# Optimization experiments

Hardware: AMD Instinct MI355X
Metric: run time of the kernel (lower is better)

## Reference

```python
import jax, jax.numpy as jnp
import numpy as np

TOP_K = 3
THRESH = 0.2
# scales=[1] -> multi_scale_fft reduces to one full-length window:
# combined_amplitudes = |rfft(x, axis=1)|.mean(channels)

def setup_inputs() -> dict:
    key = jax.random.key(0)
    x = jax.random.normal(key, (64, 4096, 64), dtype=jnp.float32)
    return {"x": x}

def _autocorr_score(xi, p):
    # xi: [T, C]; p: scalar int32 period (guaranteed in [2, T//2]).
    # Equivalent to mean over consecutive period-segments i of
    # cosine_similarity(flatten(seg_i), flatten(seg_{i+1})) — computed via
    # prefix sums of lag-p cross products so the segment reshape never needs
    # a data-dependent shape.
    T, C = xi.shape
    t = jnp.arange(T)
    tp = t + p
    m = (tp < T).astype(xi.dtype)
    xs = xi[jnp.clip(tp, 0, T - 1)]                  # [T, C] rows shifted by p
    r = (xi * xs).sum(-1) * m                        # <x[t], x[t+p]>
    q = (xi * xi).sum(-1)                            # ||x[t]||^2
    z = jnp.zeros((1,), xi.dtype)
    CR = jnp.concatenate([z, jnp.cumsum(r)])         # [T+1]
    CQ = jnp.concatenate([z, jnp.cumsum(q)])
    nper = T // p
    i = jnp.arange(T // 2)                           # max possible segments (p>=2)
    seg = i < (nper - 1)
    s = jnp.clip(i * p, 0, T)
    e = jnp.clip((i + 1) * p, 0, T)
    e2 = jnp.clip((i + 2) * p, 0, T)
    dots = CR[e] - CR[s]                             # flat dot(seg_i, seg_{i+1})
    na = jnp.sqrt(jnp.maximum(CQ[e] - CQ[s], 0.0))
    nb = jnp.sqrt(jnp.maximum(CQ[e2] - CQ[e], 0.0))
    cos = dots / jnp.maximum(na * nb, 1e-8)          # F.cosine_similarity eps
    denom = jnp.maximum(nper - 1, 1).astype(xi.dtype)
    score = jnp.where(seg, cos, 0.0).sum() / denom
    return jnp.where(nper >= 2, score, 0.0)

def reference(x):
    B, T, C = x.shape
    half = T // 2
    # multi-scale FFT with scales=[1]: single window == full sequence
    amps = jnp.abs(jnp.fft.rfft(x, axis=1)).mean(-1)       # [B, T//2+1]
    _, idx = jax.lax.top_k(amps, 2 * TOP_K)                 # [B, 2K]
    period_f = T / (idx + 1).astype(jnp.float32)            # candidate periods
    in_range = (period_f >= 2.0) & (period_f <= half)       # float-period filter
    p_int = jnp.clip(jnp.floor(period_f).astype(jnp.int32), 2, half)
    pf_floor = jnp.floor(period_f)
    in_range_int = (pf_floor >= 2.0) & (pf_floor <= half)   # int-period filter
    # autocorrelation validation score per (batch, candidate)
    scores = jax.vmap(lambda xi, ps: jax.vmap(lambda p: _autocorr_score(xi, p))(ps))(x, p_int)  # [B, 2K]
    valid = in_range & in_range_int & (scores > THRESH)
    # deterministic fallback periods (torch.randint branch unreachable for TOP_K=3)
    common = np.array([T // 4, T // 3, T // 2, int(T / 1.5)], dtype=np.int32)
    common = common[(common >= 2) & (common <= half)]
    add = jnp.asarray(common)                               # [>= TOP_K]

    def select(p_row, v_row):
        order = jnp.argsort(jnp.logical_not(v_row), stable=True)  # valid first, order kept
        sp = p_row[order][:TOP_K]
        cnt = jnp.minimum(v_row.sum(), TOP_K)
        j = jnp.arange(TOP_K)
        filled = jnp.where(j < cnt, sp, add[jnp.clip(j - cnt, 0, add.shape[0] - 1)])
        w = jnp.where(j < cnt, 1.0, 0.5)
        return filled.astype(jnp.float32), w.astype(jnp.float32)

    periods, weights = jax.vmap(select)(p_int, valid)       # [B, TOP_K] each
    return periods, weights
```

## Files before the change

### kernel.cpp

```cpp
#include <hip/hip_runtime.h>
#include <math.h>

#define T_LEN 4096
#define C_CH 64
#define B_N 64
#define NBINS 2049
#define K2 6
#define TOPK 3
#define THRESH_V 0.2f

#define PIDX(i) ((i) + ((i) >> 5))
#define ZSZ (T_LEN + (T_LEN >> 5))

__device__ __forceinline__ unsigned short f2bf(float v) {
    unsigned int u = __float_as_uint(v);
    u += 0x7FFFu + ((u >> 16) & 1u);
    return (unsigned short)(u >> 16);
}
__device__ __forceinline__ float bf2f(unsigned short h) {
    return __uint_as_float(((unsigned int)h) << 16);
}
__device__ __forceinline__ float2 zld(unsigned int v) {
    return make_float2(__uint_as_float(v << 16), __uint_as_float(v & 0xFFFF0000u));
}
__device__ __forceinline__ unsigned int zst(float2 z) {
    return (unsigned int)f2bf(z.x) | ((unsigned int)f2bf(z.y) << 16);
}

__device__ __forceinline__ float2 cmul(float2 a, float2 b) {
    return make_float2(a.x * b.x - a.y * b.y, a.x * b.y + a.y * b.x);
}
__device__ __forceinline__ float2 cadd(float2 a, float2 b) { return make_float2(a.x + b.x, a.y + b.y); }
__device__ __forceinline__ float2 csub(float2 a, float2 b) { return make_float2(a.x - b.x, a.y - b.y); }

__device__ __forceinline__ void dft16(float2* v) {
    const float C2 = 0.70710678118654752f;
    const float C1 = 0.92387953251128676f;
    const float S1 = 0.38268343236508977f;
    const int br[16] = {0, 8, 4, 12, 2, 10, 6, 14, 1, 9, 5, 13, 3, 11, 7, 15};
    float2 a[16];
#pragma unroll
    for (int i = 0; i < 16; ++i) a[i] = v[br[i]];
#pragma unroll
    for (int g = 0; g < 16; g += 2) {
        float2 t = a[g + 1];
        a[g + 1] = csub(a[g], t);
        a[g] = cadd(a[g], t);
    }
#pragma unroll
    for (int g = 0; g < 16; g += 4) {
        {
            float2 t = a[g + 2];
            a[g + 2] = csub(a[g], t);
            a[g] = cadd(a[g], t);
        }
        {
            float2 t = make_float2(a[g + 3].y, -a[g + 3].x);
            a[g + 3] = csub(a[g + 1], t);
            a[g + 1] = cadd(a[g + 1], t);
        }
    }
    {
        const float2 W4[4] = {{1.f, 0.f}, {C2, -C2}, {0.f, -1.f}, {-C2, -C2}};
#pragma unroll
        for (int g = 0; g < 16; g += 8)
#pragma unroll
            for (int j = 0; j < 4; ++j) {
                float2 t = cmul(W4[j], a[g + 4 + j]);
                a[g + 4 + j] = csub(a[g + j], t);
                a[g + j] = cadd(a[g + j], t);
            }
    }
    {
        const float2 W8[8] = {{1.f, 0.f}, {C1, -S1}, {C2, -C2}, {S1, -C1},
                              {0.f, -1.f}, {-S1, -C1}, {-C2, -C2}, {-C1, -S1}};
#pragma unroll
        for (int j = 0; j < 8; ++j) {
            float2 t = cmul(W8[j], a[8 + j]);
            a[8 + j] = csub(a[j], t);
            a[j] = cadd(a[j], t);
        }
    }
#pragma unroll
    for (int i = 0; i < 16; ++i) v[i] = a[i];
}

__global__ void transpose_cvt_kernel(const float* __restrict__ x,
                                     unsigned short* __restrict__ xtbf,
                                     float* __restrict__ amps) {
    __shared__ float tile[64][65];
    const int b = blockIdx.y;
    const int t0 = blockIdx.x * 64;
    const int lane = threadIdx.x & 63;
    const int w = threadIdx.x >> 6;
    {
        const int blin = blockIdx.y * (T_LEN / 64) + blockIdx.x;
        if (threadIdx.x < 34) {
            int idx = blin * 34 + threadIdx.x;
            if (idx < B_N * NBINS) amps[idx] = 0.f;
        }
    }
    const float* xb = x + (size_t)b * T_LEN * C_CH;
#pragma unroll
    for (int i = 0; i < 16; ++i) {
        int r = w * 16 + i;
        tile[r][lane] = xb[(size_t)(t0 + r) * C_CH + lane];
    }
    __syncthreads();
    const int half = lane >> 5;
    const int tc = (lane & 31) * 2;
#pragma unroll
    for (int it = 0; it < 8; ++it) {
        int c = it * 8 + w * 2 + half;
        float v0 = tile[tc][c];
        float v1 = tile[tc + 1][c];
        unsigned int o = (unsigned int)f2bf(v0) | ((unsigned int)f2bf(v1) << 16);
        unsigned int* dst = (unsigned int*)(xtbf + ((size_t)b * C_CH + c) * T_LEN + t0);
        dst[lane & 31] = o;
    }
}

template <int MODE>
__launch_bounds__(256, 8)
__global__ void fft_amp_kernel(const void* __restrict__ srcv, float* __restrict__ amps) {
    __shared__ unsigned int Z[ZSZ];
    const int pair = blockIdx.x;
    const int b = blockIdx.y;
    const int tid = threadIdx.x;

    if (MODE == 0) {
        const unsigned short* r0 =
            (const unsigned short*)srcv + ((size_t)b * C_CH + pair * 2) * T_LEN;
        const unsigned short* r1 = r0 + T_LEN;
#pragma unroll
        for (int k = 0; k < 2; ++k) {
            int t0 = k * 2048 + tid * 8;
            uint4 u0 = *(const uint4*)(r0 + t0);
            uint4 u1 = *(const uint4*)(r1 + t0);
            unsigned int a[4] = {u0.x, u0.y, u0.z, u0.w};
            unsigned int c[4] = {u1.x, u1.y, u1.z, u1.w};
#pragma unroll
            for (int j = 0; j < 4; ++j) {
                Z[PIDX(t0 + 2 * j)] = (a[j] & 0xFFFFu) | (c[j] << 16);
                Z[PIDX(t0 + 2 * j + 1)] = (a[j] >> 16) | (c[j] & 0xFFFF0000u);
            }
        }
    } else {
        const float* x = (const float*)srcv;
        const int c0 = pair * 2;
        for (int t = tid; t < T_LEN; t += 256) {
            float2 v = *(const float2*)(x + ((size_t)b * T_LEN + t) * C_CH + c0);
            Z[PIDX(t)] = zst(v);
        }
    }
    __syncthreads();

    {
        float2 v[16];
#pragma unroll
        for (int t = 0; t < 16; ++t) v[t] = zld(Z[PIDX(tid + 256 * t)]);
        dft16(v);
        float s, c;
        __sincosf(-(float)tid * 1.5339807878856412e-3f, &s, &c);
        float2 w1 = make_float2(c, s), w = w1;
#pragma unroll
        for (int r = 1; r < 16; ++r) {
            v[r] = cmul(v[r], w);
            w = cmul(w, w1);
        }
#pragma unroll
        for (int r = 0; r < 16; ++r) Z[PIDX(256 * r + tid)] = zst(v[r]);
    }
    __syncthreads();

    {
        const int r = tid >> 4, mu = tid & 15;
        float2 v[16];
#pragma unroll
        for (int nu = 0; nu < 16; ++nu) v[nu] = zld(Z[PIDX(256 * r + mu + 16 * nu)]);
        dft16(v);
        float s, c;
        __sincosf(-(float)mu * 2.4543692606170259e-2f, &s, &c);
        float2 w1 = make_float2(c, s), w = w1;
#pragma unroll
        for (int rho = 1; rho < 16; ++rho) {
            v[rho] = cmul(v[rho], w);
            w = cmul(w, w1);
        }
#pragma unroll
        for (int rho = 0; rho < 16; ++rho) Z[PIDX(256 * r + mu + 16 * rho)] = zst(v[rho]);
    }
    __builtin_amdgcn_wave_barrier();

    {
        const int r = tid >> 4, rho = tid & 15;
        float2 v[16];
#pragma unroll
        for (int mu = 0; mu < 16; ++mu) v[mu] = zld(Z[PIDX(256 * r + mu + 16 * rho)]);
        dft16(v);
#pragma unroll
        for (int mp = 0; mp < 16; ++mp) Z[PIDX(256 * r + mp + 16 * rho)] = zst(v[mp]);
    }
    __syncthreads();

    for (int k = tid; k < NBINS; k += 256) {
        int km = (T_LEN - k) & (T_LEN - 1);
        int sk = 256 * (k & 15) + 16 * ((k >> 4) & 15) + (k >> 8);
        int sm = 256 * (km & 15) + 16 * ((km >> 4) & 15) + (km >> 8);
        float2 zk = zld(Z[PIDX(sk)]);
        float2 zm = zld(Z[PIDX(sm)]);
        float ax = 0.5f * (zk.x + zm.x);
        float ay = 0.5f * (zk.y - zm.y);
        float bx = 0.5f * (zk.y + zm.y);
        float by = -0.5f * (zk.x - zm.x);
        float amp = sqrtf(ax * ax + ay * ay) + sqrtf(bx * bx + by * by);
        atomicAdd(&amps[(size_t)b * NBINS + k], amp);
    }
}

__global__ void topk_kernel(const float* __restrict__ amps, int* __restrict__ p_int,
                            int* __restrict__ preval, int* __restrict__ counter) {
    __shared__ float vals[NBINS];
    __shared__ float sval[256];
    __shared__ int sidx[256];
    __shared__ int sel[K2];
    const int b = blockIdx.x;
    const int tid = threadIdx.x;
    if (b == 0 && tid == 0) *counter = 0;
    for (int k = tid; k < NBINS; k += 256) vals[k] = amps[(size_t)b * NBINS + k];
    __syncthreads();
    for (int pass = 0; pass < K2; ++pass) {
        float bv = -INFINITY;
        int bi = NBINS;
        for (int k = tid; k < NBINS; k += 256) {
            float v = vals[k];
            if (v > bv || (v == bv && k < bi)) { bv = v; bi = k; }
        }
        sval[tid] = bv;
        sidx[tid] = bi;
        __syncthreads();
        for (int off = 128; off > 0; off >>= 1) {
            if (tid < off) {
                float ov = sval[tid + off];
                int oi = sidx[tid + off];
                if (ov > sval[tid] || (ov == sval[tid] && oi < sidx[tid])) {
                    sval[tid] = ov;
                    sidx[tid] = oi;
                }
            }
            __syncthreads();
        }
        if (tid == 0) {
            sel[pass] = sidx[0];
            vals[sidx[0]] = -INFINITY;
        }
        __syncthreads();
    }
    if (tid < K2) {
        int idx = sel[tid];
        float pf = (float)T_LEN / (float)(idx + 1);
        int ir = (pf >= 2.0f) && (pf <= (float)(T_LEN / 2));
        float pff = floorf(pf);
        int iri = (pff >= 2.0f) && (pff <= (float)(T_LEN / 2));
        int pi = (int)pff;
        pi = pi < 2 ? 2 : (pi > T_LEN / 2 ? T_LEN / 2 : pi);
        p_int[b * K2 + tid] = pi;
        preval[b * K2 + tid] = ir && iri;
    }
}

__global__ void rq_kernel(const unsigned short* __restrict__ xtbf,
                          const int* __restrict__ p_int, float* __restrict__ r_ws,
                          float* __restrict__ q_ws) {
    const int b = blockIdx.y;
    const int t = blockIdx.x * 64 + threadIdx.x;
    const unsigned short* xb = xtbf + (size_t)b * C_CH * T_LEN;

    int tpc[K2];
    float m[K2];
#pragma unroll
    for (int j = 0; j < K2; ++j) {
        int tp = t + p_int[b * K2 + j];
        m[j] = (tp < T_LEN) ? 1.f : 0.f;
        tpc[j] = (tp < T_LEN) ? tp : (T_LEN - 1);
    }

    float qacc = 0.f;
    float racc[K2] = {0.f, 0.f, 0.f, 0.f, 0.f, 0.f};
    for (int cc = 0; cc < C_CH; cc += 8) {
        float a[8];
        float bv[K2][8];
#pragma unroll
        for (int k = 0; k < 8; ++k) a[k] = bf2f(xb[(size_t)(cc + k) * T_LEN + t]);
#pragma unroll
        for (int j = 0; j < K2; ++j)
#pragma unroll
            for (int k = 0; k < 8; ++k)
                bv[j][k] = bf2f(xb[(size_t)(cc + k) * T_LEN + tpc[j]]);
#pragma unroll
        for (int k = 0; k < 8; ++k) {
            qacc += a[k] * a[k];
#pragma unroll
            for (int j = 0; j < K2; ++j) racc[j] += a[k] * bv[j][k];
        }
    }
    q_ws[(size_t)b * T_LEN + t] = qacc;
#pragma unroll
    for (int j = 0; j < K2; ++j)
        r_ws[((size_t)b * K2 + j) * T_LEN + t] = racc[j] * m[j];
}

__device__ __forceinline__ void block_scan2_4096(float* a, float* b, float* tsa, float* tsb,
                                                 int tid) {
    float la[16], lb[16];
    const int base = tid * 16;
    float sa = 0.f, sb = 0.f;
#pragma unroll
    for (int i = 0; i < 16; ++i) {
        sa += a[base + i];
        la[i] = sa;
        sb += b[base + i];
        lb[i] = sb;
    }
    tsa[tid] = sa;
    tsb[tid] = sb;
    __syncthreads();
    for (int off = 1; off < 256; off <<= 1) {
        float va = (tid >= off) ? tsa[tid - off] : 0.f;
        float vb = (tid >= off) ? tsb[tid - off] : 0.f;
        __syncthreads();
        tsa[tid] += va;
        tsb[tid] += vb;
        __syncthreads();
    }
    float offa = tsa[tid] - sa;
    float offb = tsb[tid] - sb;
#pragma unroll
    for (int i = 0; i < 16; ++i) {
        a[base + i] = offa + la[i];
        b[base + i] = offb + lb[i];
    }
    __syncthreads();
}

__device__ __forceinline__ void block_scan_4096(float* a, float* tsum, int tid) {
    float loc[16];
    const int base = tid * 16;
    float s = 0.f;
#pragma unroll
    for (int i = 0; i < 16; ++i) {
        s += a[base + i];
        loc[i] = s;
    }
    tsum[tid] = s;
    __syncthreads();
    for (int off = 1; off < 256; off <<= 1) {
        float v = (tid >= off) ? tsum[tid - off] : 0.f;
        __syncthreads();
        tsum[tid] += v;
        __syncthreads();
    }
    float offs = tsum[tid] - s;
#pragma unroll
    for (int i = 0; i < 16; ++i) a[base + i] = offs + loc[i];
    __syncthreads();
}

__device__ __forceinline__ void select_core(int b, const int* p_int, const int* preval,
                                            const float* sc6, float* out) {
    int sel[TOPK];
    int cnt = 0;
    for (int j = 0; j < K2; ++j) {
        if (preval[b * K2 + j] && sc6[j] > THRESH_V) {
            if (cnt < TOPK) sel[cnt] = p_int[b * K2 + j];
            cnt++;
        }
    }
    if (cnt > TOPK) cnt = TOPK;
    int add[4];
    int nadd = 0;
    int cms[4] = {T_LEN / 4, T_LEN / 3, T_LEN / 2, (int)((float)T_LEN / 1.5f)};
    for (int i = 0; i < 4; ++i)
        if (cms[i] >= 2 && cms[i] <= T_LEN / 2) add[nadd++] = cms[i];
    for (int j = 0; j < TOPK; ++j) {
        float pv, wv;
        if (j < cnt) {
            pv = (float)sel[j];
            wv = 1.0f;
        } else {
            int a = j - cnt;
            if (a > nadd - 1) a = nadd - 1;
            pv = (float)add[a];
            wv = 0.5f;
        }
        out[b * TOPK + j] = pv;
        out[B_N * TOPK + b * TOPK + j] = wv;
    }
}

__global__ void score_kernel(const float* __restrict__ r_ws, const float* __restrict__ q_ws,
                             const int* __restrict__ p_int, const int* __restrict__ preval,
                             float* __restrict__ scores, int* __restrict__ counter,
                             float* __restrict__ out) {
    __shared__ float r_s[T_LEN];
    __shared__ float q_s[T_LEN];
    __shared__ float tsum[512];
    __shared__ int lastflag;
    const int cand = blockIdx.x;
    const int b = blockIdx.y;
    const int tid = threadIdx.x;
    const int p = p_int[b * K2 + cand];
    const float4* rsrc = (const float4*)(r_ws + ((size_t)b * K2 + cand) * T_LEN);
    const float4* qsrc = (const float4*)(q_ws + (size_t)b * T_LEN);
    for (int i = tid; i < T_LEN / 4; i += 256) {
        ((float4*)r_s)[i] = rsrc[i];
        ((float4*)q_s)[i] = qsrc[i];
    }
    __syncthreads();
    block_scan2_4096(r_s, q_s, tsum, tsum + 256, tid);
    const int nper = T_LEN / p;
    float part = 0.f;
    for (int i = tid; i < nper - 1; i += 256) {
        int s0 = i * p;
        int e = s0 + p;
        int e2 = e + p;
        float crs = s0 ? r_s[s0 - 1] : 0.f;
        float dots = r_s[e - 1] - crs;
        float cqs = s0 ? q_s[s0 - 1] : 0.f;
        float qa = q_s[e - 1] - cqs;
        float qb = q_s[e2 - 1] - q_s[e - 1];
        float na = sqrtf(fmaxf(qa, 0.f));
        float nb = sqrtf(fmaxf(qb, 0.f));
        part += dots / fmaxf(na * nb, 1e-8f);
    }
    tsum[tid] = part;
    __syncthreads();
    for (int off = 128; off > 0; off >>= 1) {
        if (tid < off) tsum[tid] += tsum[tid + off];
        __syncthreads();
    }
    if (tid == 0) {
        float sc = tsum[0] / (float)(nper - 1);
        float old = atomicExch(&scores[b * K2 + cand], sc);
        int inc;
        asm volatile("v_mov_b32 %0, 1" : "=v"(inc) : "v"(old));
        int prev = atomicAdd(counter, inc);
        lastflag = (prev == K2 * B_N - 1) ? 1 : 0;
    }
    __syncthreads();
    if (lastflag && tid < B_N) {
        float sc6[K2];
#pragma unroll
        for (int j = 0; j < K2; ++j)
            sc6[j] = atomicAdd(&scores[tid * K2 + j], 0.0f);
        select_core(tid, p_int, preval, sc6, out);
    }
}

__global__ void autocorr_kernel(const float* __restrict__ x, const int* __restrict__ p_int,
                                float* __restrict__ scores) {
    __shared__ float r_s[T_LEN];
    __shared__ float q_s[T_LEN];
    __shared__ float tsum[256];
    const int cand = blockIdx.x;
    const int b = blockIdx.y;
    const int tid = threadIdx.x;
    const int p = p_int[b * K2 + cand];
    const float* xb = x + (size_t)b * T_LEN * C_CH;
    for (int t = tid; t < T_LEN; t += 256) {
        const float4* row = (const float4*)(xb + (size_t)t * C_CH);
        float q = 0.f, r = 0.f;
        if (t + p < T_LEN) {
            const float4* row2 = (const float4*)(xb + (size_t)(t + p) * C_CH);
#pragma unroll
            for (int i = 0; i < 16; ++i) {
                float4 a = row[i], c = row2[i];
                r += a.x * c.x + a.y * c.y + a.z * c.z + a.w * c.w;
                q += a.x * a.x + a.y * a.y + a.z * a.z + a.w * a.w;
            }
        } else {
#pragma unroll
            for (int i = 0; i < 16; ++i) {
                float4 a = row[i];
                q += a.x * a.x + a.y * a.y + a.z * a.z + a.w * a.w;
            }
        }
        r_s[t] = r;
        q_s[t] = q;
    }
    __syncthreads();
    block_scan_4096(r_s, tsum, tid);
    block_scan_4096(q_s, tsum, tid);
    const int nper = T_LEN / p;
    float part = 0.f;
    for (int i = tid; i < nper - 1; i += 256) {
        int s0 = i * p;
        int e = s0 + p;
        int e2 = e + p;
        float crs = s0 ? r_s[s0 - 1] : 0.f;
        float dots = r_s[e - 1] - crs;
        float cqs = s0 ? q_s[s0 - 1] : 0.f;
        float qa = q_s[e - 1] - cqs;
        float qb = q_s[e2 - 1] - q_s[e - 1];
        float na = sqrtf(fmaxf(qa, 0.f));
        float nb = sqrtf(fmaxf(qb, 0.f));
        part += dots / fmaxf(na * nb, 1e-8f);
    }
    tsum[tid] = part;
    __syncthreads();
    for (int off = 128; off > 0; off >>= 1) {
        if (tid < off) tsum[tid] += tsum[tid + off];
        __syncthreads();
    }
    if (tid == 0) scores[b * K2 + cand] = tsum[0] / (float)(nper - 1);
}

__global__ void select_kernel(const int* __restrict__ p_int, const int* __restrict__ preval,
                              const float* __restrict__ scores, float* __restrict__ out) {
    const int b = threadIdx.x;
    if (b >= B_N) return;
    float sc6[K2];
    for (int j = 0; j < K2; ++j) sc6[j] = scores[b * K2 + j];
    select_core(b, p_int, preval, sc6, out);
}

static size_t align256(size_t v) { return (v + 255) & ~(size_t)255; }

extern "C" void kernel_launch(void* const* d_in, const int* in_sizes, int n_in,
                              void* d_out, int out_size, void* d_ws, size_t ws_size,
                              hipStream_t stream) {
    const float* x = (const float*)d_in[0];
    float* out = (float*)d_out;
    char* ws = (char*)d_ws;

    const size_t amps_b = align256((size_t)B_N * NBINS * sizeof(float));
    const size_t int_b = align256((size_t)B_N * K2 * sizeof(int));
    const size_t r_b = align256((size_t)B_N * K2 * T_LEN * sizeof(float));
    const size_t q_b = align256((size_t)B_N * T_LEN * sizeof(float));
    const size_t xtbf_b = align256((size_t)B_N * T_LEN * C_CH * sizeof(short));

    size_t off = 0;
    float* amps = (float*)(ws + off); off += amps_b;
    int* p_int = (int*)(ws + off); off += int_b;
    int* preval = (int*)(ws + off); off += int_b;
    float* scores = (float*)(ws + off); off += int_b;
    int* counter = (int*)(ws + off); off += 256;
    float* r_ws = (float*)(ws + off); off += r_b;
    float* q_ws = (float*)(ws + off); off += q_b;
    unsigned short* xtbf = (unsigned short*)(ws + off); off += xtbf_b;
    const size_t full_need = off;

    if (ws_size >= full_need) {
        transpose_cvt_kernel<<<dim3(T_LEN / 64, B_N), 256, 0, stream>>>(x, xtbf, amps);
        fft_amp_kernel<0><<<dim3(C_CH / 2, B_N), 256, 0, stream>>>(xtbf, amps);
        topk_kernel<<<B_N, 256, 0, stream>>>(amps, p_int, preval, counter);
        rq_kernel<<<dim3(T_LEN / 64, B_N), 64, 0, stream>>>(xtbf, p_int, r_ws, q_ws);
        score_kernel<<<dim3(K2, B_N), 256, 0, stream>>>(r_ws, q_ws, p_int, preval, scores,
                                                        counter, out);
    } else {
        hipMemsetAsync(amps, 0, amps_b, stream);
        fft_amp_kernel<1><<<dim3(C_CH / 2, B_N), 256, 0, stream>>>(x, amps);
        topk_kernel<<<B_N, 256, 0, stream>>>(amps, p_int, preval, counter);
        autocorr_kernel<<<dim3(K2, B_N), 256, 0, stream>>>(x, p_int, scores);
        select_kernel<<<1, 64, 0, stream>>>(p_int, preval, scores, out);
    }
}
```

Baseline: 166.8 us.

## Fuse top-k selection into FFT kernel via per-batch last-block counter

Removes the separate topk kernel launch on the main path. Each FFT block atomically bumps a per-batch counter, and the last of the 32 channel-pair blocks for a batch reloads the accumulated amplitudes into shared memory and runs the top-k selection there. Counters are zeroed in the transpose kernel, and the score kernel's counter logic is rewritten to use a separate slot with a barrier. This saves a launch and an intermediate pass, but it serializes the top-k work onto one tail block per batch, and correctness depends on the atomic amplitude adds being visible without an explicit fence.

```diff
diff --git a/kernel.cpp b/kernel.cpp
--- a/kernel.cpp
+++ b/kernel.cpp
@@ -85,9 +85,51 @@
     for (int i = 0; i < 16; ++i) v[i] = a[i];
 }
 
+__device__ __forceinline__ void topk_select(float* vals, float* sval, int* sidx, int* sel,
+                                            int b, int tid, int* p_int, int* preval) {
+    for (int pass = 0; pass < K2; ++pass) {
+        float bv = -INFINITY;
+        int bi = NBINS;
+        for (int k = tid; k < NBINS; k += 256) {
+            float v = vals[k];
+            if (v > bv || (v == bv && k < bi)) { bv = v; bi = k; }
+        }
+        sval[tid] = bv;
+        sidx[tid] = bi;
+        __syncthreads();
+        for (int off = 128; off > 0; off >>= 1) {
+            if (tid < off) {
+                float ov = sval[tid + off];
+                int oi = sidx[tid + off];
+                if (ov > sval[tid] || (ov == sval[tid] && oi < sidx[tid])) {
+                    sval[tid] = ov;
+                    sidx[tid] = oi;
+                }
+            }
+            __syncthreads();
+        }
+        if (tid == 0) {
+            sel[pass] = sidx[0];
+            vals[sidx[0]] = -INFINITY;
+        }
+        __syncthreads();
+    }
+    if (tid < K2) {
+        int idx = sel[tid];
+        float pf = (float)T_LEN / (float)(idx + 1);
+        int ir = (pf >= 2.0f) && (pf <= (float)(T_LEN / 2));
+        float pff = floorf(pf);
+        int iri = (pff >= 2.0f) && (pff <= (float)(T_LEN / 2));
+        int pi = (int)pff;
+        pi = pi < 2 ? 2 : (pi > T_LEN / 2 ? T_LEN / 2 : pi);
+        p_int[b * K2 + tid] = pi;
+        preval[b * K2 + tid] = ir && iri;
+    }
+}
+
 __global__ void transpose_cvt_kernel(const float* __restrict__ x,
                                      unsigned short* __restrict__ xtbf,
-                                     float* __restrict__ amps) {
+                                     float* __restrict__ amps, int* __restrict__ cnts) {
     __shared__ float tile[64][65];
     const int b = blockIdx.y;
     const int t0 = blockIdx.x * 64;
@@ -99,6 +141,7 @@
             int idx = blin * 34 + threadIdx.x;
             if (idx < B_N * NBINS) amps[idx] = 0.f;
         }
+        if (blin == 0 && threadIdx.x < B_N + 1) cnts[threadIdx.x] = 0;
     }
     const float* xb = x + (size_t)b * T_LEN * C_CH;
 #pragma unroll
@@ -122,8 +165,11 @@
 
 template <int MODE>
 __launch_bounds__(256, 8)
-__global__ void fft_amp_kernel(const void* __restrict__ srcv, float* __restrict__ amps) {
+__global__ void fft_amp_kernel(const void* __restrict__ srcv, float* __restrict__ amps,
+                               int* __restrict__ cnts, int* __restrict__ p_int,
+                               int* __restrict__ preval) {
     __shared__ unsigned int Z[ZSZ];
+    __shared__ int lastflag;
     const int pair = blockIdx.x;
     const int b = blockIdx.y;
     const int tid = threadIdx.x;
@@ -216,6 +262,22 @@
         float amp = sqrtf(ax * ax + ay * ay) + sqrtf(bx * bx + by * by);
         atomicAdd(&amps[(size_t)b * NBINS + k], amp);
     }
+
+    if (MODE != 0) return;
+
+    __syncthreads();
+    if (tid == 0) lastflag = (atomicAdd(&cnts[b], 1) == 31) ? 1 : 0;
+    __syncthreads();
+    if (!lastflag) return;
+
+    float* vals = (float*)Z;
+    float* sval = vals + NBINS;
+    int* sidx = (int*)(sval + 256);
+    int* sel = sidx + 256;
+    for (int k = tid; k < NBINS; k += 256)
+        vals[k] = atomicAdd(&amps[(size_t)b * NBINS + k], 0.0f);
+    __syncthreads();
+    topk_select(vals, sval, sidx, sel, b, tid, p_int, preval);
 }
 
 __global__ void topk_kernel(const float* __restrict__ amps, int* __restrict__ p_int,
@@ -229,44 +291,7 @@
     if (b == 0 && tid == 0) *counter = 0;
     for (int k = tid; k < NBINS; k += 256) vals[k] = amps[(size_t)b * NBINS + k];
     __syncthreads();
-    for (int pass = 0; pass < K2; ++pass) {
-        float bv = -INFINITY;
-        int bi = NBINS;
-        for (int k = tid; k < NBINS; k += 256) {
-            float v = vals[k];
-            if (v > bv || (v == bv && k < bi)) { bv = v; bi = k; }
-        }
-        sval[tid] = bv;
-        sidx[tid] = bi;
-        __syncthreads();
-        for (int off = 128; off > 0; off >>= 1) {
-            if (tid < off) {
-                float ov = sval[tid + off];
-                int oi = sidx[tid + off];
-                if (ov > sval[tid] || (ov == sval[tid] && oi < sidx[tid])) {
-                    sval[tid] = ov;
-                    sidx[tid] = oi;
-                }
-            }
-            __syncthreads();
-        }
-        if (tid == 0) {
-            sel[pass] = sidx[0];
-            vals[sidx[0]] = -INFINITY;
-        }
-        __syncthreads();
-    }
-    if (tid < K2) {
-        int idx = sel[tid];
-        float pf = (float)T_LEN / (float)(idx + 1);
-        int ir = (pf >= 2.0f) && (pf <= (float)(T_LEN / 2));
-        float pff = floorf(pf);
-        int iri = (pff >= 2.0f) && (pff <= (float)(T_LEN / 2));
-        int pi = (int)pff;
-        pi = pi < 2 ? 2 : (pi > T_LEN / 2 ? T_LEN / 2 : pi);
-        p_int[b * K2 + tid] = pi;
-        preval[b * K2 + tid] = ir && iri;
-    }
+    topk_select(vals, sval, sidx, sel, b, tid, p_int, preval);
 }
 
 __global__ void rq_kernel(const unsigned short* __restrict__ xtbf,
@@ -441,12 +466,10 @@
     }
     if (tid == 0) {
         float sc = tsum[0] / (float)(nper - 1);
-        float old = atomicExch(&scores[b * K2 + cand], sc);
-        int inc;
-        asm volatile("v_mov_b32 %0, 1" : "=v"(inc) : "v"(old));
-        int prev = atomicAdd(counter, inc);
-        lastflag = (prev == K2 * B_N - 1) ? 1 : 0;
-    }
+        atomicExch(&scores[b * K2 + cand], sc);
+    }
+    __syncthreads();
+    if (tid == 0) lastflag = (atomicAdd(counter, 1) == K2 * B_N - 1) ? 1 : 0;
     __syncthreads();
     if (lastflag && tid < B_N) {
         float sc6[K2];
@@ -535,6 +558,7 @@
 
     const size_t amps_b = align256((size_t)B_N * NBINS * sizeof(float));
     const size_t int_b = align256((size_t)B_N * K2 * sizeof(int));
+    const size_t cnt_b = align256((size_t)(B_N + 1) * sizeof(int));
     const size_t r_b = align256((size_t)B_N * K2 * T_LEN * sizeof(float));
     const size_t q_b = align256((size_t)B_N * T_LEN * sizeof(float));
     const size_t xtbf_b = align256((size_t)B_N * T_LEN * C_CH * sizeof(short));
@@ -544,23 +568,24 @@
     int* p_int = (int*)(ws + off); off += int_b;
     int* preval = (int*)(ws + off); off += int_b;
     float* scores = (float*)(ws + off); off += int_b;
-    int* counter = (int*)(ws + off); off += 256;
+    int* cnts = (int*)(ws + off); off += cnt_b;
     float* r_ws = (float*)(ws + off); off += r_b;
     float* q_ws = (float*)(ws + off); off += q_b;
     unsigned short* xtbf = (unsigned short*)(ws + off); off += xtbf_b;
     const size_t full_need = off;
 
     if (ws_size >= full_need) {
-        transpose_cvt_kernel<<<dim3(T_LEN / 64, B_N), 256, 0, stream>>>(x, xtbf, amps);
-        fft_amp_kernel<0><<<dim3(C_CH / 2, B_N), 256, 0, stream>>>(xtbf, amps);
-        topk_kernel<<<B_N, 256, 0, stream>>>(amps, p_int, preval, counter);
+        transpose_cvt_kernel<<<dim3(T_LEN / 64, B_N), 256, 0, stream>>>(x, xtbf, amps, cnts);
+        fft_amp_kernel<0><<<dim3(C_CH / 2, B_N), 256, 0, stream>>>(xtbf, amps, cnts, p_int,
+                                                                   preval);
         rq_kernel<<<dim3(T_LEN / 64, B_N), 64, 0, stream>>>(xtbf, p_int, r_ws, q_ws);
         score_kernel<<<dim3(K2, B_N), 256, 0, stream>>>(r_ws, q_ws, p_int, preval, scores,
-                                                        counter, out);
+                                                        &cnts[B_N], out);
     } else {
         hipMemsetAsync(amps, 0, amps_b, stream);
-        fft_amp_kernel<1><<<dim3(C_CH / 2, B_N), 256, 0, stream>>>(x, amps);
-        topk_kernel<<<B_N, 256, 0, stream>>>(amps, p_int, preval, counter);
+        fft_amp_kernel<1><<<dim3(C_CH / 2, B_N), 256, 0, stream>>>(x, amps, cnts, p_int,
+                                                                   preval);
+        topk_kernel<<<B_N, 256, 0, stream>>>(amps, p_int, preval, &cnts[B_N]);
         autocorr_kernel<<<dim3(K2, B_N), 256, 0, stream>>>(x, p_int, scores);
         select_kernel<<<1, 64, 0, stream>>>(p_int, preval, scores, out);
     }
```

After: 176.5 us. +5.9%, slower.
